# Optimization experiments

Measured on AMD Instinct MI355X. Metric: run time of the kernel, lower is better.

## Reference

```python
import jax, jax.numpy as jnp
import numpy as np

N, C, F = 2048, 512, 512

def setup_inputs() -> dict:
    key = jax.random.key(0)
    k1, k2 = jax.random.split(key)
    x = jax.random.normal(k1, (N, F), dtype=jnp.float32)
    means = jax.random.normal(k2, (C, F), dtype=jnp.float32)
    return {"x": x, "means": means}

def reference(x, means):
    # Negative squared Euclidean distance from each sample to each class mean.
    # diff: (N, C, F) broadcasted; output: (N, C)
    diff = x[:, None, :] - means[None, :, :]
    return -jnp.sum(diff * diff, axis=-1)
```

## Files before the change

kernel.cpp:

```cpp
#include <hip/hip_runtime.h>
#include <hip/hip_bf16.h>
#include <string.h>


#define F_DIM  512
#define C_ROWS 512

typedef __attribute__((ext_vector_type(8))) short short8;
typedef __attribute__((ext_vector_type(4))) float f32x4;

static __device__ __forceinline__ unsigned pk_bf16(float lo, float hi) {
    __hip_bfloat162 h = __float22bfloat162_rn(make_float2(lo, hi));
    unsigned u;
    memcpy(&u, &h, 4);
    return u;
}

__global__ __launch_bounds__(512) void ncm_fused(
        const float* __restrict__ x, const float* __restrict__ means,
        float* __restrict__ out) {
    __shared__ __align__(16) short As[64 * 512];
    __shared__ __align__(16) short Bs[64 * 512];
    __shared__ float xn_s[64], mn_s[64];

    const int d  = blockIdx.x;
    const int by = (d & 7) * 4 + ((d >> 3) & 3);
    const int bx = d >> 5;
    const int rowBase = by * 64, colBase = bx * 64;

    const int t    = threadIdx.x;
    const int w    = t >> 6;
    const int lane = t & 63;
    const int qr   = lane >> 4;
    const int ql   = lane & 15;

    float4 va[2][2][4][2];
#pragma unroll
    for (int half = 0; half < 2; half++) {
        const float* src = (half == 0) ? x + (size_t)rowBase * F_DIM
                                       : means + (size_t)colBase * F_DIM;
#pragma unroll
        for (int i = 0; i < 2; i++) {
            const float* rowp = src + (size_t)(w * 8 + i * 4 + qr) * F_DIM;
#pragma unroll
            for (int ph = 0; ph < 4; ph++) {
                const float* p = rowp + ph * 128 + ql * 8;
                va[half][i][ph][0] = *(const float4*)p;
                va[half][i][ph][1] = *(const float4*)(p + 4);
            }
        }
    }

#pragma unroll
    for (int half = 0; half < 2; half++) {
        short* dst  = (half == 0) ? As : Bs;
        float* nrm  = (half == 0) ? xn_s : mn_s;
#pragma unroll
        for (int i = 0; i < 2; i++) {
            const int r = w * 8 + i * 4 + qr;
            float ss = 0.f;
#pragma unroll
            for (int ph = 0; ph < 4; ph++) {
                float vv[8] = {va[half][i][ph][0].x, va[half][i][ph][0].y,
                               va[half][i][ph][0].z, va[half][i][ph][0].w,
                               va[half][i][ph][1].x, va[half][i][ph][1].y,
                               va[half][i][ph][1].z, va[half][i][ph][1].w};
                int4 o;
                o.x = (int)pk_bf16(vv[0], vv[1]);
                o.y = (int)pk_bf16(vv[2], vv[3]);
                o.z = (int)pk_bf16(vv[4], vv[5]);
                o.w = (int)pk_bf16(vv[6], vv[7]);
#pragma unroll
                for (int j = 0; j < 8; j++) ss += vv[j] * vv[j];
                const int slot = ph * 16 + ql;
                *(int4*)(dst + r * F_DIM + ((slot ^ (r & 7)) << 3)) = o;
            }
            ss += __shfl_xor(ss, 1);
            ss += __shfl_xor(ss, 2);
            ss += __shfl_xor(ss, 4);
            ss += __shfl_xor(ss, 8);
            if (ql == 0) nrm[r] = ss;
        }
    }
    __syncthreads();

    const int quad = w & 3;
    const int kh   = w >> 2;
    const int wr   = (quad >> 1) * 32;
    const int wc   = (quad & 1) * 32;

    f32x4 acc[2][2];
#pragma unroll
    for (int mi = 0; mi < 2; mi++)
#pragma unroll
        for (int ni = 0; ni < 2; ni++)
            acc[mi][ni] = (f32x4){0.f, 0.f, 0.f, 0.f};

#pragma unroll
    for (int j = 0; j < 8; j++) {
        const int kk   = kh * 8 + j;
        const int slot = kk * 4 + (lane >> 4);
        short8 a[2], b[2];
#pragma unroll
        for (int mi = 0; mi < 2; mi++) {
            const int r = wr + mi * 16 + (lane & 15);
            a[mi] = *(const short8*)(As + r * F_DIM + ((slot ^ (r & 7)) << 3));
        }
#pragma unroll
        for (int ni = 0; ni < 2; ni++) {
            const int r = wc + ni * 16 + (lane & 15);
            b[ni] = *(const short8*)(Bs + r * F_DIM + ((slot ^ (r & 7)) << 3));
        }
#pragma unroll
        for (int mi = 0; mi < 2; mi++)
#pragma unroll
            for (int ni = 0; ni < 2; ni++)
                acc[mi][ni] = __builtin_amdgcn_mfma_f32_16x16x32_bf16(
                    a[mi], b[ni], acc[mi][ni], 0, 0, 0);
    }

    __syncthreads();
    float* red = (float*)As;
    if (kh == 1) {
#pragma unroll
        for (int mi = 0; mi < 2; mi++)
#pragma unroll
            for (int ni = 0; ni < 2; ni++)
#pragma unroll
                for (int j = 0; j < 4; j++)
                    red[quad * 1088 + lane * 17 + mi * 8 + ni * 4 + j] =
                        acc[mi][ni][j];
    }
    __syncthreads();
    if (kh == 0) {
#pragma unroll
        for (int mi = 0; mi < 2; mi++)
#pragma unroll
            for (int ni = 0; ni < 2; ni++)
#pragma unroll
                for (int j = 0; j < 4; j++)
                    acc[mi][ni][j] +=
                        red[quad * 1088 + lane * 17 + mi * 8 + ni * 4 + j];

        float xn[2][4];
#pragma unroll
        for (int mi = 0; mi < 2; mi++)
#pragma unroll
            for (int j = 0; j < 4; j++)
                xn[mi][j] = xn_s[wr + mi * 16 + (lane >> 4) * 4 + j];

#pragma unroll
        for (int ni = 0; ni < 2; ni++) {
            const int cl = wc + ni * 16 + (lane & 15);
            const int c  = colBase + cl;
            const float mn = mn_s[cl];
#pragma unroll
            for (int mi = 0; mi < 2; mi++) {
                const int rbase = rowBase + wr + mi * 16 + (lane >> 4) * 4;
#pragma unroll
                for (int j = 0; j < 4; j++)
                    out[(size_t)(rbase + j) * C_ROWS + c] =
                        2.0f * acc[mi][ni][j] - xn[mi][j] - mn;
            }
        }
    }
}

extern "C" void kernel_launch(void* const* d_in, const int* in_sizes, int n_in,
                              void* d_out, int out_size, void* d_ws, size_t ws_size,
                              hipStream_t stream) {
    const float* x     = (const float*)d_in[0];
    const float* means = (const float*)d_in[1];
    float* out = (float*)d_out;
    ncm_fused<<<256, 512, 0, stream>>>(x, means, out);
}
```

Before: 12.21 us.

## Split bf16 conversion into prep kernel and stream tiles via global_load_lds

The single fused kernel is split into two. A prep kernel converts x and means to bf16 once, writing a swizzled layout and row norms into workspace. The GEMM kernel then fills its LDS tiles with direct global_load_lds copies of half-width data, so the redundant per-block fp32 loading and conversion goes away. In exchange it adds a second launch and a workspace round trip, and it falls back to a slow naive kernel when the workspace is too small.

```diff
diff --git a/kernel.cpp b/kernel.cpp
--- a/kernel.cpp
+++ b/kernel.cpp
@@ -3,8 +3,9 @@
 #include <string.h>
 
 
+#define N_ROWS 2048
+#define C_ROWS 512
 #define F_DIM  512
-#define C_ROWS 512
 
 typedef __attribute__((ext_vector_type(8))) short short8;
 typedef __attribute__((ext_vector_type(4))) float f32x4;
@@ -16,8 +17,54 @@
     return u;
 }
 
-__global__ __launch_bounds__(512) void ncm_fused(
+__global__ __launch_bounds__(256) void prep_kernel(
         const float* __restrict__ x, const float* __restrict__ means,
+        short* __restrict__ xb, short* __restrict__ mb,
+        float* __restrict__ xnorm, float* __restrict__ mnorm) {
+    const int w    = threadIdx.x >> 6;
+    const int lane = threadIdx.x & 63;
+    const int row  = blockIdx.x * 4 + w;
+
+    const float* src;
+    short* dst;
+    float* nrm;
+    int rk;
+    if (row < N_ROWS) {
+        src = x + (size_t)row * F_DIM;
+        dst = xb + (size_t)row * F_DIM;
+        nrm = xnorm + row;
+        rk  = row & 7;
+    } else {
+        const int r = row - N_ROWS;
+        src = means + (size_t)r * F_DIM;
+        dst = mb + (size_t)r * F_DIM;
+        nrm = mnorm + r;
+        rk  = r & 7;
+    }
+
+    float4 v0 = *(const float4*)(src + lane * 8);
+    float4 v1 = *(const float4*)(src + lane * 8 + 4);
+    float vv[8] = {v0.x, v0.y, v0.z, v0.w, v1.x, v1.y, v1.z, v1.w};
+
+    float ss = 0.f;
+#pragma unroll
+    for (int j = 0; j < 8; j++) ss += vv[j] * vv[j];
+
+    int4 o;
+    o.x = (int)pk_bf16(vv[0], vv[1]);
+    o.y = (int)pk_bf16(vv[2], vv[3]);
+    o.z = (int)pk_bf16(vv[4], vv[5]);
+    o.w = (int)pk_bf16(vv[6], vv[7]);
+    *(int4*)(dst + ((lane ^ rk) << 3)) = o;
+
+#pragma unroll
+    for (int off = 32; off > 0; off >>= 1) ss += __shfl_xor(ss, off);
+    if (lane == 0) *nrm = ss;
+}
+
+__global__ __launch_bounds__(512) void nsq_gemm(
+        const short* __restrict__ xb, const short* __restrict__ mb,
+        const float* __restrict__ xnorm, const float* __restrict__ mnorm,
         float* __restrict__ out) {
     __shared__ __align__(16) short As[64 * 512];
     __shared__ __align__(16) short Bs[64 * 512];
@@ -31,57 +78,24 @@
     const int t    = threadIdx.x;
     const int w    = t >> 6;
     const int lane = t & 63;
-    const int qr   = lane >> 4;
-    const int ql   = lane & 15;
-
-    float4 va[2][2][4][2];
-#pragma unroll
-    for (int half = 0; half < 2; half++) {
-        const float* src = (half == 0) ? x + (size_t)rowBase * F_DIM
-                                       : means + (size_t)colBase * F_DIM;
-#pragma unroll
-        for (int i = 0; i < 2; i++) {
-            const float* rowp = src + (size_t)(w * 8 + i * 4 + qr) * F_DIM;
-#pragma unroll
-            for (int ph = 0; ph < 4; ph++) {
-                const float* p = rowp + ph * 128 + ql * 8;
-                va[half][i][ph][0] = *(const float4*)p;
-                va[half][i][ph][1] = *(const float4*)(p + 4);
-            }
-        }
-    }
-
-#pragma unroll
-    for (int half = 0; half < 2; half++) {
-        short* dst  = (half == 0) ? As : Bs;
-        float* nrm  = (half == 0) ? xn_s : mn_s;
-#pragma unroll
-        for (int i = 0; i < 2; i++) {
-            const int r = w * 8 + i * 4 + qr;
-            float ss = 0.f;
-#pragma unroll
-            for (int ph = 0; ph < 4; ph++) {
-                float vv[8] = {va[half][i][ph][0].x, va[half][i][ph][0].y,
-                               va[half][i][ph][0].z, va[half][i][ph][0].w,
-                               va[half][i][ph][1].x, va[half][i][ph][1].y,
-                               va[half][i][ph][1].z, va[half][i][ph][1].w};
-                int4 o;
-                o.x = (int)pk_bf16(vv[0], vv[1]);
-                o.y = (int)pk_bf16(vv[2], vv[3]);
-                o.z = (int)pk_bf16(vv[4], vv[5]);
-                o.w = (int)pk_bf16(vv[6], vv[7]);
-#pragma unroll
-                for (int j = 0; j < 8; j++) ss += vv[j] * vv[j];
-                const int slot = ph * 16 + ql;
-                *(int4*)(dst + r * F_DIM + ((slot ^ (r & 7)) << 3)) = o;
-            }
-            ss += __shfl_xor(ss, 1);
-            ss += __shfl_xor(ss, 2);
-            ss += __shfl_xor(ss, 4);
-            ss += __shfl_xor(ss, 8);
-            if (ql == 0) nrm[r] = ss;
-        }
-    }
+
+    const short* ga = xb + (size_t)rowBase * F_DIM;
+    const short* gb = mb + (size_t)colBase * F_DIM;
+#pragma unroll
+    for (int i = 0; i < 8; i++) {
+        const short* srcA = ga + ((size_t)(i * 512 + t) << 3);
+        const short* srcB = gb + ((size_t)(i * 512 + t) << 3);
+        short* la = As + i * 4096 + w * 512;
+        short* lb = Bs + i * 4096 + w * 512;
+        __builtin_amdgcn_global_load_lds(
+            (const __attribute__((address_space(1))) void*)srcA,
+            (__attribute__((address_space(3))) void*)la, 16, 0, 0);
+        __builtin_amdgcn_global_load_lds(
+            (const __attribute__((address_space(1))) void*)srcB,
+            (__attribute__((address_space(3))) void*)lb, 16, 0, 0);
+    }
+    if (t < 64)       xn_s[t]      = xnorm[rowBase + t];
+    else if (t < 128) mn_s[t - 64] = mnorm[colBase + (t - 64)];
     __syncthreads();
 
     const int quad = w & 3;
@@ -164,6 +178,23 @@
             }
         }
     }
+}
+
+__global__ __launch_bounds__(256) void fallback_kernel(
+        const float* __restrict__ x, const float* __restrict__ means,
+        float* __restrict__ out) {
+    __shared__ float xrow[F_DIM];
+    const int n = blockIdx.x;
+    const int c = blockIdx.y * 256 + threadIdx.x;
+    for (int f = threadIdx.x; f < F_DIM; f += 256) xrow[f] = x[(size_t)n * F_DIM + f];
+    __syncthreads();
+    const float* m = means + (size_t)c * F_DIM;
+    float s = 0.f;
+    for (int f = 0; f < F_DIM; f++) {
+        float d = xrow[f] - m[f];
+        s += d * d;
+    }
+    out[(size_t)n * C_ROWS + c] = -s;
 }
 
 extern "C" void kernel_launch(void* const* d_in, const int* in_sizes, int n_in,
@@ -172,5 +203,20 @@
     const float* x     = (const float*)d_in[0];
     const float* means = (const float*)d_in[1];
     float* out = (float*)d_out;
-    ncm_fused<<<256, 512, 0, stream>>>(x, means, out);
-}
+
+    const size_t need = (size_t)N_ROWS * F_DIM * 2 + (size_t)C_ROWS * F_DIM * 2 +
+                        (size_t)(N_ROWS + C_ROWS) * 4;
+    if (ws_size >= need) {
+        short* xb = (short*)d_ws;
+        short* mb = xb + (size_t)N_ROWS * F_DIM;
+        float* xnorm = (float*)(mb + (size_t)C_ROWS * F_DIM);
+        float* mnorm = xnorm + N_ROWS;
+
+        prep_kernel<<<(N_ROWS + C_ROWS) / 4, 256, 0, stream>>>(
+            x, means, xb, mb, xnorm, mnorm);
+        nsq_gemm<<<256, 512, 0, stream>>>(xb, mb, xnorm, mnorm, out);
+    } else {
+        dim3 grid(N_ROWS, C_ROWS / 256);
+        fallback_kernel<<<grid, 256, 0, stream>>>(x, means, out);
+    }
+}
```

After: 15.02 us. +23.1%, slower.

## Double block size to 1024 threads with 4-way split-K and vectorized reduction

Applied to the files above, without the earlier changes.

Raises the block from 512 to 1024 threads, so each wave loads and converts only one operand half and K is split four ways across wave groups instead of two. The cross-group reduction now uses swizzled float4 LDS stores and loads instead of scalar padded accesses. The aim is more memory-level parallelism and shorter per-wave MFMA chains within the same 256-block grid. In exchange, the register budget per thread shrinks and the reduction adds more LDS traffic and a larger serial summation on the kh==0 waves.

```diff
diff --git a/kernel.cpp b/kernel.cpp
--- a/kernel.cpp
+++ b/kernel.cpp
@@ -16,7 +16,7 @@
     return u;
 }
 
-__global__ __launch_bounds__(512) void ncm_fused(
+__global__ __launch_bounds__(1024) void ncm_fused(
         const float* __restrict__ x, const float* __restrict__ means,
         float* __restrict__ out) {
     __shared__ __align__(16) short As[64 * 512];
@@ -34,44 +34,37 @@
     const int qr   = lane >> 4;
     const int ql   = lane & 15;
 
-    float4 va[2][2][4][2];
-#pragma unroll
-    for (int half = 0; half < 2; half++) {
+    {
+        const int half  = w >> 3;
+        const int wrow8 = (w & 7) * 8;
         const float* src = (half == 0) ? x + (size_t)rowBase * F_DIM
                                        : means + (size_t)colBase * F_DIM;
+        short* dst = (half == 0) ? As : Bs;
+        float* nrm = (half == 0) ? xn_s : mn_s;
+
 #pragma unroll
         for (int i = 0; i < 2; i++) {
-            const float* rowp = src + (size_t)(w * 8 + i * 4 + qr) * F_DIM;
+            const int r = wrow8 + i * 4 + qr;
+            const float* rowp = src + (size_t)r * F_DIM;
+            float4 va[4][2];
 #pragma unroll
             for (int ph = 0; ph < 4; ph++) {
                 const float* p = rowp + ph * 128 + ql * 8;
-                va[half][i][ph][0] = *(const float4*)p;
-                va[half][i][ph][1] = *(const float4*)(p + 4);
+                va[ph][0] = *(const float4*)p;
+                va[ph][1] = *(const float4*)(p + 4);
             }
-        }
-    }
-
-#pragma unroll
-    for (int half = 0; half < 2; half++) {
-        short* dst  = (half == 0) ? As : Bs;
-        float* nrm  = (half == 0) ? xn_s : mn_s;
-#pragma unroll
-        for (int i = 0; i < 2; i++) {
-            const int r = w * 8 + i * 4 + qr;
             float ss = 0.f;
 #pragma unroll
             for (int ph = 0; ph < 4; ph++) {
-                float vv[8] = {va[half][i][ph][0].x, va[half][i][ph][0].y,
-                               va[half][i][ph][0].z, va[half][i][ph][0].w,
-                               va[half][i][ph][1].x, va[half][i][ph][1].y,
-                               va[half][i][ph][1].z, va[half][i][ph][1].w};
+                float vv[8] = {va[ph][0].x, va[ph][0].y, va[ph][0].z, va[ph][0].w,
+                               va[ph][1].x, va[ph][1].y, va[ph][1].z, va[ph][1].w};
+#pragma unroll
+                for (int j = 0; j < 8; j++) ss += vv[j] * vv[j];
                 int4 o;
                 o.x = (int)pk_bf16(vv[0], vv[1]);
                 o.y = (int)pk_bf16(vv[2], vv[3]);
                 o.z = (int)pk_bf16(vv[4], vv[5]);
                 o.w = (int)pk_bf16(vv[6], vv[7]);
-#pragma unroll
-                for (int j = 0; j < 8; j++) ss += vv[j] * vv[j];
                 const int slot = ph * 16 + ql;
                 *(int4*)(dst + r * F_DIM + ((slot ^ (r & 7)) << 3)) = o;
             }
@@ -97,8 +90,8 @@
             acc[mi][ni] = (f32x4){0.f, 0.f, 0.f, 0.f};
 
 #pragma unroll
-    for (int j = 0; j < 8; j++) {
-        const int kk   = kh * 8 + j;
+    for (int j = 0; j < 4; j++) {
+        const int kk   = kh * 4 + j;
         const int slot = kk * 4 + (lane >> 4);
         short8 a[2], b[2];
 #pragma unroll
@@ -121,26 +114,28 @@
 
     __syncthreads();
     float* red = (float*)As;
-    if (kh == 1) {
+    if (kh > 0) {
+        const int g = kh - 1;
+        float* base = red + (g * 4 + quad) * 1024 + lane * 16;
 #pragma unroll
-        for (int mi = 0; mi < 2; mi++)
-#pragma unroll
-            for (int ni = 0; ni < 2; ni++)
-#pragma unroll
-                for (int j = 0; j < 4; j++)
-                    red[quad * 1088 + lane * 17 + mi * 8 + ni * 4 + j] =
-                        acc[mi][ni][j];
+        for (int s = 0; s < 4; s++) {
+            const int sw = s ^ ((lane >> 1) & 3);
+            *(f32x4*)(base + sw * 4) = acc[s >> 1][s & 1];
+        }
     }
     __syncthreads();
     if (kh == 0) {
 #pragma unroll
-        for (int mi = 0; mi < 2; mi++)
+        for (int g = 0; g < 3; g++) {
+            const float* base = red + (g * 4 + quad) * 1024 + lane * 16;
 #pragma unroll
-            for (int ni = 0; ni < 2; ni++)
+            for (int s = 0; s < 4; s++) {
+                const int sw = s ^ ((lane >> 1) & 3);
+                f32x4 v = *(const f32x4*)(base + sw * 4);
 #pragma unroll
-                for (int j = 0; j < 4; j++)
-                    acc[mi][ni][j] +=
-                        red[quad * 1088 + lane * 17 + mi * 8 + ni * 4 + j];
+                for (int j = 0; j < 4; j++) acc[s >> 1][s & 1][j] += v[j];
+            }
+        }
 
         float xn[2][4];
 #pragma unroll
@@ -172,5 +167,5 @@
     const float* x     = (const float*)d_in[0];
     const float* means = (const float*)d_in[1];
     float* out = (float*)d_out;
-    ncm_fused<<<256, 512, 0, stream>>>(x, means, out);
+    ncm_fused<<<256, 1024, 0, stream>>>(x, means, out);
 }
```

After: 11.62 us. -4.8%, faster.
